# Kernel optimization log

Measured on AMD Instinct MI355X. Metric: run time of the kernel, lower is better.

## Reference

```python
import jax, jax.numpy as jnp
import numpy as np
import math

N, E, D, H = 1536, 49152, 512, 8
DH = D // H  # head dim = 64
SCALE = 256.0 * math.sqrt(2.0)  # rel_dists scaling in forward


def sinusoidal_pe(x, d):
    """x: [...] float positions -> [..., d] interleaved sin/cos encoding."""
    div = jnp.exp(jnp.arange(0, d, 2, dtype=jnp.float32) * (-math.log(10000.0) / d))
    ang = x[..., None] * div  # [..., d//2]
    return jnp.stack([jnp.sin(ang), jnp.cos(ang)], axis=-1).reshape(*x.shape, d)


def setup_inputs() -> dict:
    key = jax.random.key(0)
    ks = jax.random.split(key, 8)
    features = jax.random.normal(ks[0], (N, D), dtype=jnp.float32)
    edge_index = jax.random.randint(ks[1], (2, E), 0, N, dtype=jnp.int64)
    edge_attr = jax.random.uniform(ks[2], (E,), dtype=jnp.float32)  # normalized distances
    pos = jax.random.uniform(ks[3], (N, 2), dtype=jnp.float32)  # unused by forward
    s = 1.0 / math.sqrt(D)  # ~xavier-uniform bound sqrt(6/(D+D))... use simple symmetric init
    Wq = jax.random.uniform(ks[4], (D, D), minval=-s, maxval=s, dtype=jnp.float32)
    Wk = jax.random.uniform(ks[5], (D, D), minval=-s, maxval=s, dtype=jnp.float32)
    Wv = jax.random.uniform(ks[6], (D, D), minval=-s, maxval=s, dtype=jnp.float32)
    bq = jnp.zeros((D,), jnp.float32)
    bk = jnp.zeros((D,), jnp.float32)
    bv = jnp.zeros((D,), jnp.float32)
    return dict(features=features, edge_index=edge_index, edge_attr=edge_attr, pos=pos,
                Wq=Wq, bq=bq, Wk=Wk, bk=bk, Wv=Wv, bv=bv)


def reference(features, edge_index, edge_attr, pos, Wq, bq, Wk, bk, Wv, bv):
    # batch dim is 1 in the original (features.unsqueeze(0)); we omit it.
    q = (features @ Wq.T + bq).reshape(N, H, DH).transpose(1, 0, 2)  # [H,N,DH]
    k = (features @ Wk.T + bk).reshape(N, H, DH).transpose(1, 0, 2)
    v = (features @ Wv.T + bv).reshape(N, H, DH).transpose(1, 0, 2)

    qk = jnp.einsum('hqd,hrd->hqr', q, k)  # [H,N,N]

    # to_dense_adj: scatter-add edge_attr into dense [N,N], then scale
    rel = jnp.zeros((N, N), jnp.float32).at[edge_index[0], edge_index[1]].add(edge_attr) * SCALE
    # embed_k and embed_q are identical parameter-free sinusoidal encodings of rel
    rk = sinusoidal_pe(rel, DH)  # [N,N,DH]

    # original: qk + q.rk + k.rq + (q_repeat*k_repeat == qk)  => 2*qk + q.rk + k.rk
    logits = 2.0 * qk \
        + jnp.einsum('hqd,qrd->hqr', q, rk) \
        + jnp.einsum('hrd,qrd->hqr', k, rk)
    attn = jax.nn.softmax(logits / math.sqrt(DH), axis=-1)  # [H,N,N]

    out = jnp.einsum('hqr,hrd->hqd', attn, v)  # [H,N,DH]
    out = out.transpose(1, 0, 2).reshape(N, D)  # [N,D]
    return out.max(axis=0)  # [D] max-pool over nodes (MIL pooling)
```

## Files before the change

### kernel.cpp

```cpp
#include <hip/hip_runtime.h>
#include <cmath>


constexpr int Nn  = 1536;
constexpr int Dd  = 512;
constexpr int Hh  = 8;
constexpr int DHd = 64;
constexpr int SPLITS = 4;
constexpr float SCALE_F = 362.03867196751236f;
constexpr float M0 = 8.0f;

typedef float f4 __attribute__((ext_vector_type(4)));
typedef int   i4 __attribute__((ext_vector_type(4)));
typedef __attribute__((ext_vector_type(4))) float f32x4;
typedef __attribute__((ext_vector_type(8))) short bf16x8;

__device__ inline unsigned short bf16_rne(float x) {
    unsigned u = __float_as_uint(x);
    unsigned r = u + 0x7fff + ((u >> 16) & 1);
    return (unsigned short)(r >> 16);
}
__device__ inline float bf16_tof(unsigned short h) {
    return __uint_as_float(((unsigned)h) << 16);
}
__device__ inline unsigned f2ord(float x) {
    unsigned b = __float_as_uint(x);
    return (b & 0x80000000u) ? ~b : (b | 0x80000000u);
}

__global__ __launch_bounds__(256) void pack_fw_k(
    const float* __restrict__ feat,
    const float* __restrict__ Wq, const float* __restrict__ Wk, const float* __restrict__ Wv,
    unsigned short* __restrict__ pFh, unsigned short* __restrict__ pFl,
    unsigned short* __restrict__ pWh, unsigned short* __restrict__ pWl)
{
    int tg = blockIdx.x * 256 + threadIdx.x;
    int type = blockIdx.y;
    int L = tg & 63;
    int kc = (tg >> 6) & 15;
    int t10 = tg >> 10;
    const float* src;
    unsigned short *oh, *ol;
    int row, col;
    if (type == 0) {
        src = feat; oh = pFh; ol = pFl;
        row = t10 * 16 + (L & 15);
        col = kc * 32 + (L >> 4) * 8;
    } else {
        int z = t10 >> 5, nt = t10 & 31;
        src = (z == 0) ? Wq : (z == 1) ? Wk : Wv;
        oh = pWh; ol = pWl;
        row = nt * 16 + (L & 15);
        col = kc * 32 + (L >> 4) * 8;
    }
    f4 a = *(const f4*)(src + (size_t)row * Dd + col);
    f4 b = *(const f4*)(src + (size_t)row * Dd + col + 4);
    float x[8];
    #pragma unroll
    for (int j = 0; j < 4; ++j) { x[j] = a[j]; x[4 + j] = b[j]; }
    unsigned short hs[8], ls[8];
    #pragma unroll
    for (int j = 0; j < 8; ++j) {
        hs[j] = bf16_rne(x[j]);
        ls[j] = bf16_rne(x[j] - bf16_tof(hs[j]));
    }
    *(bf16x8*)(oh + (size_t)tg * 8) = *(bf16x8*)hs;
    *(bf16x8*)(ol + (size_t)tg * 8) = *(bf16x8*)ls;
}

__global__ __launch_bounds__(256) void qkvm_k(
    const unsigned short* __restrict__ pFh, const unsigned short* __restrict__ pFl,
    const unsigned short* __restrict__ pWh, const unsigned short* __restrict__ pWl,
    const float* __restrict__ bq, const float* __restrict__ bk, const float* __restrict__ bv,
    float* __restrict__ Qo, float* __restrict__ Ko,
    unsigned short* __restrict__ pQh, unsigned short* __restrict__ pQl,
    unsigned short* __restrict__ pKh, unsigned short* __restrict__ pKl,
    unsigned short* __restrict__ pVh, unsigned short* __restrict__ pVl)
{
    const int z = blockIdx.z;
    const float* __restrict__ bias = (z == 0) ? bq : (z == 1) ? bk : bv;
    const int tid = threadIdx.x;
    const int L = tid & 63, wv = tid >> 6;
    const int l15 = L & 15, quad = L >> 4;
    const int mt0 = blockIdx.y * 4 + (wv & 1) * 2;
    const int nt0 = blockIdx.x * 4 + (wv >> 1) * 2;
    __shared__ float lds[4][32][33];

    f32x4 acc[2][2];
    #pragma unroll
    for (int i = 0; i < 2; ++i)
        #pragma unroll
        for (int j = 0; j < 2; ++j) acc[i][j] = (f32x4){0.f, 0.f, 0.f, 0.f};

    bf16x8 AH[2][2], AL[2][2], BH[2][2], BL[2][2];
    auto loadset = [&](int buf, int kc) {
        #pragma unroll
        for (int i = 0; i < 2; ++i) {
            size_t ao = ((size_t)((mt0 + i) * 16 + kc)) * 512 + L * 8;
            AH[buf][i] = *(const bf16x8*)(pFh + ao);
            AL[buf][i] = *(const bf16x8*)(pFl + ao);
            size_t bo = ((size_t)((z * 32 + nt0 + i) * 16 + kc)) * 512 + L * 8;
            BH[buf][i] = *(const bf16x8*)(pWh + bo);
            BL[buf][i] = *(const bf16x8*)(pWl + bo);
        }
    };
    auto mfmaset = [&](int buf) {
        #pragma unroll
        for (int i = 0; i < 2; ++i)
            #pragma unroll
            for (int j = 0; j < 2; ++j) {
                f32x4 a = acc[i][j];
                a = __builtin_amdgcn_mfma_f32_16x16x32_bf16(AH[buf][i], BH[buf][j], a, 0, 0, 0);
                a = __builtin_amdgcn_mfma_f32_16x16x32_bf16(AH[buf][i], BL[buf][j], a, 0, 0, 0);
                a = __builtin_amdgcn_mfma_f32_16x16x32_bf16(AL[buf][i], BH[buf][j], a, 0, 0, 0);
                a = __builtin_amdgcn_mfma_f32_16x16x32_bf16(AL[buf][i], BL[buf][j], a, 0, 0, 0);
                acc[i][j] = a;
            }
    };

    loadset(0, 0);
    #pragma unroll
    for (int kc = 0; kc < 16; kc += 2) {
        loadset(1, kc + 1);
        mfmaset(0);
        if (kc + 2 < 16) loadset(0, kc + 2);
        mfmaset(1);
    }

    float o_[2][2][4];
    #pragma unroll
    for (int i = 0; i < 2; ++i)
        #pragma unroll
        for (int j = 0; j < 2; ++j) {
            float b = bias[(nt0 + j) * 16 + l15];
            #pragma unroll
            for (int reg = 0; reg < 4; ++reg) o_[i][j][reg] = acc[i][j][reg] + b;
        }
    if (z < 2) {
        float* __restrict__ outp = (z == 0) ? Qo : Ko;
        #pragma unroll
        for (int i = 0; i < 2; ++i) {
            int row0 = (mt0 + i) * 16 + quad * 4;
            #pragma unroll
            for (int j = 0; j < 2; ++j) {
                int col = (nt0 + j) * 16 + l15;
                #pragma unroll
                for (int reg = 0; reg < 4; ++reg)
                    outp[(size_t)(row0 + reg) * Dd + col] = o_[i][j][reg];
            }
        }
    }
    #pragma unroll
    for (int i = 0; i < 2; ++i)
        #pragma unroll
        for (int j = 0; j < 2; ++j)
            #pragma unroll
            for (int reg = 0; reg < 4; ++reg)
                lds[wv][i * 16 + quad * 4 + reg][j * 16 + l15] = o_[i][j][reg];

    const int h = blockIdx.x;
    if (z < 2) {
        unsigned short* __restrict__ oh = z ? pKh : pQh;
        unsigned short* __restrict__ ol = z ? pKl : pQl;
        const int kc = wv >> 1;
        const float sc = z ? 1.0f : 0.25f;
        #pragma unroll
        for (int i = 0; i < 2; ++i) {
            float x[8]; unsigned short hs[8], ls[8];
            #pragma unroll
            for (int j2 = 0; j2 < 8; ++j2)
                x[j2] = lds[wv][i * 16 + l15][quad * 8 + j2] * sc;
            #pragma unroll
            for (int j2 = 0; j2 < 8; ++j2) {
                hs[j2] = bf16_rne(x[j2]);
                ls[j2] = bf16_rne(x[j2] - bf16_tof(hs[j2]));
            }
            size_t off = ((size_t)((h * 96 + mt0 + i) * 2 + kc)) * 512 + L * 8;
            *(bf16x8*)(oh + off) = *(bf16x8*)hs;
            *(bf16x8*)(ol + off) = *(bf16x8*)ls;
        }
    } else {
        const int rc = blockIdx.y * 2 + (wv & 1);
        #pragma unroll
        for (int dtl = 0; dtl < 2; ++dtl) {
            int dt = (wv >> 1) * 2 + dtl;
            float x[8]; unsigned short hs[8], ls[8];
            #pragma unroll
            for (int j2 = 0; j2 < 8; ++j2)
                x[j2] = lds[wv][quad * 8 + j2][dtl * 16 + l15];
            #pragma unroll
            for (int j2 = 0; j2 < 8; ++j2) {
                hs[j2] = bf16_rne(x[j2]);
                ls[j2] = bf16_rne(x[j2] - bf16_tof(hs[j2]));
            }
            size_t off = ((size_t)((h * 48 + rc) * 4 + dt)) * 512 + L * 8;
            *(bf16x8*)(pVh + off) = *(bf16x8*)hs;
            *(bf16x8*)(pVl + off) = *(bf16x8*)ls;
        }
    }
}

__global__ __launch_bounds__(256) void init_rel_k(float* __restrict__ rel,
                                                  int* __restrict__ eid,
                                                  unsigned* __restrict__ ordmax)
{
    size_t idx = (size_t)blockIdx.x * 256 + threadIdx.x;
    size_t i = idx * 4;
    if (i < (size_t)Nn * Nn) {
        *(f4*)(rel + i) = (f4){0.f, 0.f, 0.f, 0.f};
        *(i4*)(eid + i) = (i4){-1, -1, -1, -1};
    }
    if (idx < 128) {
        #pragma unroll
        for (int c = 0; c < 4; ++c) ordmax[idx * 4 + c] = 0x007FFFFFu;
    }
}

__global__ __launch_bounds__(256) void scatter_k(
    const int* __restrict__ raw, const float* __restrict__ attr,
    float* __restrict__ rel, int* __restrict__ eid, int* __restrict__ idxn, int E)
{
    int e = blockIdx.x * 256 + threadIdx.x;
    if (e >= E) return;
    int acc = 0;
    #pragma unroll
    for (int i = 0; i < 16; ++i) acc |= raw[2 * i + 1];
    int s, t;
    if (acc == 0) { s = raw[2 * e]; t = raw[2 * (E + e)]; }
    else          { s = raw[e];     t = raw[E + e]; }
    idxn[e] = s; idxn[E + e] = t;
    size_t off = (size_t)s * Nn + t;
    atomicAdd(rel + off, attr[e] * SCALE_F);
    eid[off] = e;
}

__global__ void oddsum_k(const float* __restrict__ Q, const float* __restrict__ K,
                         float* __restrict__ qodd, float* __restrict__ kodd,
                         float* __restrict__ koddT)
{
    int t = blockIdx.x * 256 + threadIdx.x;
    if (t >= 2 * Nn * Hh) return;
    const float* src = (t < Nn * Hh) ? Q : K;
    int i = (t < Nn * Hh) ? t : t - Nn * Hh;
    int n = i >> 3, h = i & 7;
    const float* row = src + (size_t)n * Dd + h * DHd;
    float s = 0.f;
    #pragma unroll
    for (int ii = 0; ii < 32; ++ii) s += row[2 * ii + 1];
    if (t < Nn * Hh) qodd[i] = s;
    else { kodd[i] = s; koddT[h * Nn + n] = 0.125f * s; }
}

__global__ __launch_bounds__(256) void delta_k(
    const int* __restrict__ idxn, const float* __restrict__ rel,
    const float* __restrict__ Q, const float* __restrict__ K,
    const float* __restrict__ qodd, const float* __restrict__ kodd,
    float* __restrict__ delta8, int E)
{
    int t = blockIdx.x * 256 + threadIdx.x;
    if (t >= E * Hh) return;
    int e = t >> 3, h = t & 7;
    int qi = idxn[e], ri = idxn[E + e];
    float x = rel[(size_t)qi * Nn + ri];
    const float* qrow = Q + (size_t)qi * Dd + h * DHd;
    const float* krow = K + (size_t)ri * Dd + h * DHd;
    float acc = 0.f;
    #pragma unroll
    for (int i = 0; i < 32; i += 2) {
        float dd0 = 0.15915494309189535f * __builtin_amdgcn_exp2f(-0.4152410118609203f * (float)i);
        float dd1 = 0.15915494309189535f * __builtin_amdgcn_exp2f(-0.4152410118609203f * (float)(i + 1));
        float r0 = x * dd0; r0 -= floorf(r0);
        float r1 = x * dd1; r1 -= floorf(r1);
        float s0 = __builtin_amdgcn_sinf(r0), c0 = __builtin_amdgcn_cosf(r0);
        float s1 = __builtin_amdgcn_sinf(r1), c1 = __builtin_amdgcn_cosf(r1);
        f4 q4 = *(const f4*)(qrow + 2 * i);
        f4 k4 = *(const f4*)(krow + 2 * i);
        acc += (q4[0] + k4[0]) * s0 + (q4[1] + k4[1]) * c0
             + (q4[2] + k4[2]) * s1 + (q4[3] + k4[3]) * c1;
    }
    delta8[(size_t)e * Hh + h] = 0.125f * (acc - qodd[qi * Hh + h] - kodd[ri * Hh + h]);
}

__global__ __launch_bounds__(64, 3) void flash5_k(
    const unsigned short* __restrict__ pQh, const unsigned short* __restrict__ pQl,
    const unsigned short* __restrict__ pKh, const unsigned short* __restrict__ pKl,
    const unsigned short* __restrict__ pVh, const unsigned short* __restrict__ pVl,
    const int* __restrict__ eid, const float* __restrict__ delta8,
    const float* __restrict__ koddT,
    float* __restrict__ Opart, float* __restrict__ Lpart)
{
    const int qt = blockIdx.x, h = blockIdx.y, s = blockIdx.z;
    const int L = threadIdx.x, quad = L >> 4, l15 = L & 15;
    const int q0 = qt * 16;
    __shared__ unsigned short phi[16][80];
    __shared__ unsigned short plo[16][80];

    bf16x8 qh[2], ql[2];
    #pragma unroll
    for (int kc = 0; kc < 2; ++kc) {
        size_t off = ((size_t)((h * 96 + qt) * 2 + kc)) * 512 + L * 8;
        qh[kc] = *(const bf16x8*)(pQh + off);
        ql[kc] = *(const bf16x8*)(pQl + off);
    }

    f32x4 O[4];
    float lsum[4];
    #pragma unroll
    for (int r = 0; r < 4; ++r) { lsum[r] = 0.f; O[r] = (f32x4){0.f, 0.f, 0.f, 0.f}; }

    const int NT = 24 / SPLITS;
    const int Tbase = s * NT;

    bf16x8 kh0[4], kh1[4], kl0[4], kl1[4];
    {
        const int r0 = Tbase * 64;
        #pragma unroll
        for (int nt = 0; nt < 4; ++nt) {
            size_t b0 = ((size_t)((h * 96 + (r0 >> 4) + nt) * 2)) * 512 + L * 8;
            kh0[nt] = *(const bf16x8*)(pKh + b0);
            kh1[nt] = *(const bf16x8*)(pKh + b0 + 512);
            kl0[nt] = *(const bf16x8*)(pKl + b0);
            kl1[nt] = *(const bf16x8*)(pKl + b0 + 512);
        }
    }

    float kvcur[4], dcur[16];
    {
        const int r0 = Tbase * 64;
        int ecur[16];
        #pragma unroll
        for (int nt = 0; nt < 4; ++nt) {
            kvcur[nt] = koddT[h * Nn + r0 + nt * 16 + l15];
            #pragma unroll
            for (int reg = 0; reg < 4; ++reg)
                ecur[nt * 4 + reg] = eid[(size_t)(q0 + quad * 4 + reg) * Nn + r0 + nt * 16 + l15];
        }
        #pragma unroll
        for (int i = 0; i < 16; ++i) {
            int e = ecur[i];
            float d = delta8[(size_t)(e < 0 ? 0 : e) * Hh + h];
            dcur[i] = (e >= 0) ? d : 0.f;
        }
    }

    for (int T = 0; T < NT; ++T) {
        const int r0 = (Tbase + T) * 64;
        const bool more = (T + 1 < NT);

        int   enxt[16];
        float kvnxt[4];
        if (more) {
            const int r1 = r0 + 64;
            #pragma unroll
            for (int nt = 0; nt < 4; ++nt) {
                kvnxt[nt] = koddT[h * Nn + r1 + nt * 16 + l15];
                #pragma unroll
                for (int reg = 0; reg < 4; ++reg)
                    enxt[nt * 4 + reg] = eid[(size_t)(q0 + quad * 4 + reg) * Nn + r1 + nt * 16 + l15];
            }
        }

        bf16x8 vh0[4], vh1[4], vl0[4], vl1[4];
        #pragma unroll
        for (int dt = 0; dt < 4; ++dt) {
            size_t vb = ((size_t)((h * 48 + (r0 >> 5)) * 4 + dt)) * 512 + L * 8;
            vh0[dt] = *(const bf16x8*)(pVh + vb);
            vh1[dt] = *(const bf16x8*)(pVh + vb + 2048);
            vl0[dt] = *(const bf16x8*)(pVl + vb);
            vl1[dt] = *(const bf16x8*)(pVl + vb + 2048);
        }

        f32x4 S[4];
        #pragma unroll
        for (int nt = 0; nt < 4; ++nt) {
            f32x4 a = {0.f, 0.f, 0.f, 0.f};
            a = __builtin_amdgcn_mfma_f32_16x16x32_bf16(qh[0], kh0[nt], a, 0, 0, 0);
            a = __builtin_amdgcn_mfma_f32_16x16x32_bf16(qh[1], kh1[nt], a, 0, 0, 0);
            a = __builtin_amdgcn_mfma_f32_16x16x32_bf16(qh[0], kl0[nt], a, 0, 0, 0);
            a = __builtin_amdgcn_mfma_f32_16x16x32_bf16(qh[1], kl1[nt], a, 0, 0, 0);
            a = __builtin_amdgcn_mfma_f32_16x16x32_bf16(ql[0], kh0[nt], a, 0, 0, 0);
            a = __builtin_amdgcn_mfma_f32_16x16x32_bf16(ql[1], kh1[nt], a, 0, 0, 0);
            S[nt] = a;
        }

        if (more) {
            const int r1 = r0 + 64;
            #pragma unroll
            for (int nt = 0; nt < 4; ++nt) {
                size_t b0 = ((size_t)((h * 96 + (r1 >> 4) + nt) * 2)) * 512 + L * 8;
                kh0[nt] = *(const bf16x8*)(pKh + b0);
                kh1[nt] = *(const bf16x8*)(pKh + b0 + 512);
                kl0[nt] = *(const bf16x8*)(pKl + b0);
                kl1[nt] = *(const bf16x8*)(pKl + b0 + 512);
            }
        }

        #pragma unroll
        for (int reg = 0; reg < 4; ++reg) {
            float p[4];
            #pragma unroll
            for (int nt = 0; nt < 4; ++nt) {
                p[nt] = __expf(S[nt][reg] + kvcur[nt] + dcur[nt * 4 + reg] - M0);
                lsum[reg] += p[nt];
                unsigned short hi = bf16_rne(p[nt]);
                phi[quad * 4 + reg][nt * 16 + l15] = hi;
                plo[quad * 4 + reg][nt * 16 + l15] = bf16_rne(p[nt] - bf16_tof(hi));
            }
        }

        bf16x8 ph[2], pl[2];
        #pragma unroll
        for (int kc2 = 0; kc2 < 2; ++kc2) {
            ph[kc2] = *(const bf16x8*)&phi[l15][kc2 * 32 + quad * 8];
            pl[kc2] = *(const bf16x8*)&plo[l15][kc2 * 32 + quad * 8];
        }

        #pragma unroll
        for (int dt = 0; dt < 4; ++dt) {
            f32x4 a = O[dt];
            a = __builtin_amdgcn_mfma_f32_16x16x32_bf16(ph[0], vh0[dt], a, 0, 0, 0);
            a = __builtin_amdgcn_mfma_f32_16x16x32_bf16(ph[1], vh1[dt], a, 0, 0, 0);
            a = __builtin_amdgcn_mfma_f32_16x16x32_bf16(ph[0], vl0[dt], a, 0, 0, 0);
            a = __builtin_amdgcn_mfma_f32_16x16x32_bf16(ph[1], vl1[dt], a, 0, 0, 0);
            a = __builtin_amdgcn_mfma_f32_16x16x32_bf16(pl[0], vh0[dt], a, 0, 0, 0);
            a = __builtin_amdgcn_mfma_f32_16x16x32_bf16(pl[1], vh1[dt], a, 0, 0, 0);
            O[dt] = a;
        }

        if (more) {
            #pragma unroll
            for (int i = 0; i < 16; ++i) {
                int e = enxt[i];
                float d = delta8[(size_t)(e < 0 ? 0 : e) * Hh + h];
                dcur[i] = (e >= 0) ? d : 0.f;
            }
            #pragma unroll
            for (int nt = 0; nt < 4; ++nt) kvcur[nt] = kvnxt[nt];
        }
    }

    #pragma unroll
    for (int reg = 0; reg < 4; ++reg) {
        #pragma unroll
        for (int o = 1; o < 16; o <<= 1) lsum[reg] += __shfl_xor(lsum[reg], o);
    }

    #pragma unroll
    for (int dt = 0; dt < 4; ++dt)
        #pragma unroll
        for (int reg = 0; reg < 4; ++reg)
            Opart[((size_t)(s * Hh + h) * Nn + q0 + quad * 4 + reg) * 64 + dt * 16 + l15] = O[dt][reg];
    if (l15 == 0) {
        #pragma unroll
        for (int reg = 0; reg < 4; ++reg)
            Lpart[(size_t)(s * Hh + h) * Nn + q0 + quad * 4 + reg] = lsum[reg];
    }
}

__global__ __launch_bounds__(256) void combine_mp_k(
    const float* __restrict__ Opart, const float* __restrict__ Lpart,
    unsigned* __restrict__ ordmax)
{
    const int b = blockIdx.x;
    const int t = threadIdx.x;
    const int cg = (t & 127) * 4;
    const int h = cg >> 6, d = cg & 63;
    const int rh = t >> 7;
    f4 mx = {-3.0e38f, -3.0e38f, -3.0e38f, -3.0e38f};
    for (int r = 0; r < 8; ++r) {
        int q = b * 16 + rh * 8 + r;
        float l = 0.f;
        f4 o = {0.f, 0.f, 0.f, 0.f};
        #pragma unroll
        for (int s2 = 0; s2 < SPLITS; ++s2) {
            l += Lpart[(size_t)(s2 * Hh + h) * Nn + q];
            f4 ov = *(const f4*)(Opart + ((size_t)(s2 * Hh + h) * Nn + q) * 64 + d);
            #pragma unroll
            for (int c = 0; c < 4; ++c) o[c] += ov[c];
        }
        float inv = 1.0f / l;
        #pragma unroll
        for (int c = 0; c < 4; ++c) mx[c] = fmaxf(mx[c], o[c] * inv);
    }
    #pragma unroll
    for (int c = 0; c < 4; ++c) atomicMax(&ordmax[cg + c], f2ord(mx[c]));
}

__global__ void decode_k(const unsigned* __restrict__ ordmax, float* __restrict__ outp)
{
    int t = blockIdx.x * 256 + threadIdx.x;
    if (t >= Dd) return;
    unsigned u = ordmax[t];
    outp[t] = (u & 0x80000000u) ? __uint_as_float(u ^ 0x80000000u) : __uint_as_float(~u);
}

extern "C" void kernel_launch(void* const* d_in, const int* in_sizes, int n_in,
                              void* d_out, int out_size, void* d_ws, size_t ws_size,
                              hipStream_t stream)
{
    const float* feat   = (const float*)d_in[0];
    const int*   rawidx = (const int*)d_in[1];
    const float* attr   = (const float*)d_in[2];
    const float* Wq = (const float*)d_in[4];
    const float* bq = (const float*)d_in[5];
    const float* Wk = (const float*)d_in[6];
    const float* bk = (const float*)d_in[7];
    const float* Wv = (const float*)d_in[8];
    const float* bv = (const float*)d_in[9];
    float* outp = (float*)d_out;
    const int E = in_sizes[2];

    const size_t ND_ = (size_t)Nn * Dd;
    const size_t NN_ = (size_t)Nn * Nn;
    const size_t PK_ = (size_t)Hh * 96 * 2 * 512;
    float* ws    = (float*)d_ws;
    float* Q     = ws;
    float* K     = Q + ND_;
    unsigned short* pFh = (unsigned short*)(K + ND_);
    unsigned short* pFl = pFh + PK_;
    unsigned short* pWh = pFl + PK_;
    unsigned short* pWl = pWh + PK_;
    float* rel   = (float*)(pWl + PK_);
    int*   eid   = (int*)(rel + NN_);
    float* delta8 = (float*)(eid + NN_);
    float* qodd  = delta8 + (size_t)E * Hh;
    float* kodd  = qodd + (size_t)Nn * Hh;
    float* koddT = kodd + (size_t)Nn * Hh;
    int*   idxn  = (int*)(koddT + (size_t)Nn * Hh);
    unsigned short* pQh = (unsigned short*)(idxn + 2 * E);
    unsigned short* pQl = pQh + PK_;
    unsigned short* pKh = pQl + PK_;
    unsigned short* pKl = pKh + PK_;
    unsigned short* pVh = pKl + PK_;
    unsigned short* pVl = pVh + PK_;
    float* Lpart = (float*)(pVl + PK_);
    unsigned* ordmax = (unsigned*)(Lpart + (size_t)SPLITS * Hh * Nn);
    float* Opart = ws;

    pack_fw_k<<<dim3(384, 2), 256, 0, stream>>>(feat, Wq, Wk, Wv, pFh, pFl, pWh, pWl);
    qkvm_k<<<dim3(8, 24, 3), 256, 0, stream>>>(pFh, pFl, pWh, pWl, bq, bk, bv,
                                               Q, K, pQh, pQl, pKh, pKl, pVh, pVl);
    init_rel_k<<<(int)((NN_ / 4 + 255) / 256), 256, 0, stream>>>(rel, eid, ordmax);
    scatter_k<<<(E + 255) / 256, 256, 0, stream>>>(rawidx, attr, rel, eid, idxn, E);
    oddsum_k<<<(2 * Nn * Hh + 255) / 256, 256, 0, stream>>>(Q, K, qodd, kodd, koddT);
    delta_k<<<(E * Hh + 255) / 256, 256, 0, stream>>>(idxn, rel, Q, K, qodd, kodd, delta8, E);
    flash5_k<<<dim3(96, 8, SPLITS), 64, 0, stream>>>(pQh, pQl, pKh, pKl, pVh, pVl,
                                                     eid, delta8, koddT, Opart, Lpart);
    combine_mp_k<<<96, 256, 0, stream>>>(Opart, Lpart, ordmax);
    decode_k<<<(Dd + 255) / 256, 256, 0, stream>>>(ordmax, outp);
}
```

Baseline: 196.7 us.

## Merge init kernels, fuse odd-sums into QKV GEMM, shrink edge-id map, atomically reduce splits

Folds the pack, rel/eid init, accumulator zeroing and ordmax init into one setup kernel. The odd-lane sums move into the QKV projection epilogue as shuffle reductions plus atomics, and the separate oddsum kernel is removed. The dense edge-id map drops from int32 to uint16 to halve its init and read traffic. The flash split partials are now summed with atomicAdd into one O/L buffer, so the combine kernel no longer reads per-split partials. This removes launches and memory traffic, but adds atomic contention and relies on E fitting in 16 bits.

```diff
diff --git a/kernel.cpp b/kernel.cpp
--- a/kernel.cpp
+++ b/kernel.cpp
@@ -12,6 +12,7 @@
 
 typedef float f4 __attribute__((ext_vector_type(4)));
 typedef int   i4 __attribute__((ext_vector_type(4)));
+typedef unsigned short us4 __attribute__((ext_vector_type(4)));
 typedef __attribute__((ext_vector_type(4))) float f32x4;
 typedef __attribute__((ext_vector_type(8))) short bf16x8;
 
@@ -28,44 +29,66 @@
     return (b & 0x80000000u) ? ~b : (b | 0x80000000u);
 }
 
-__global__ __launch_bounds__(256) void pack_fw_k(
+__global__ __launch_bounds__(256) void setup_k(
     const float* __restrict__ feat,
     const float* __restrict__ Wq, const float* __restrict__ Wk, const float* __restrict__ Wv,
     unsigned short* __restrict__ pFh, unsigned short* __restrict__ pFl,
-    unsigned short* __restrict__ pWh, unsigned short* __restrict__ pWl)
-{
-    int tg = blockIdx.x * 256 + threadIdx.x;
-    int type = blockIdx.y;
-    int L = tg & 63;
-    int kc = (tg >> 6) & 15;
-    int t10 = tg >> 10;
-    const float* src;
-    unsigned short *oh, *ol;
-    int row, col;
-    if (type == 0) {
-        src = feat; oh = pFh; ol = pFl;
-        row = t10 * 16 + (L & 15);
-        col = kc * 32 + (L >> 4) * 8;
+    unsigned short* __restrict__ pWh, unsigned short* __restrict__ pWl,
+    float* __restrict__ rel, unsigned short* __restrict__ eid16,
+    float* __restrict__ Obuf, float* __restrict__ Lbuf,
+    float* __restrict__ qkodd, unsigned* __restrict__ ordmax)
+{
+    const int b = blockIdx.x, tid = threadIdx.x;
+    if (b < 768) {
+        int type = (b >= 384);
+        int tg = (type ? (b - 384) : b) * 256 + tid;
+        int L = tg & 63;
+        int kc = (tg >> 6) & 15;
+        int t10 = tg >> 10;
+        const float* src;
+        unsigned short *oh, *ol;
+        int row, col;
+        if (type == 0) {
+            src = feat; oh = pFh; ol = pFl;
+            row = t10 * 16 + (L & 15);
+            col = kc * 32 + (L >> 4) * 8;
+        } else {
+            int z = t10 >> 5, nt = t10 & 31;
+            src = (z == 0) ? Wq : (z == 1) ? Wk : Wv;
+            oh = pWh; ol = pWl;
+            row = nt * 16 + (L & 15);
+            col = kc * 32 + (L >> 4) * 8;
+        }
+        f4 a = *(const f4*)(src + (size_t)row * Dd + col);
+        f4 bb = *(const f4*)(src + (size_t)row * Dd + col + 4);
+        float x[8];
+        #pragma unroll
+        for (int j = 0; j < 4; ++j) { x[j] = a[j]; x[4 + j] = bb[j]; }
+        unsigned short hs[8], ls[8];
+        #pragma unroll
+        for (int j = 0; j < 8; ++j) {
+            hs[j] = bf16_rne(x[j]);
+            ls[j] = bf16_rne(x[j] - bf16_tof(hs[j]));
+        }
+        *(bf16x8*)(oh + (size_t)tg * 8) = *(bf16x8*)hs;
+        *(bf16x8*)(ol + (size_t)tg * 8) = *(bf16x8*)ls;
+    } else if (b < 3072) {
+        size_t idx = (size_t)(b - 768) * 256 + tid;
+        *(f4*)(rel + idx * 4) = (f4){0.f, 0.f, 0.f, 0.f};
+        *(us4*)(eid16 + idx * 4) = (us4){0xFFFFu, 0xFFFFu, 0xFFFFu, 0xFFFFu};
+    } else if (b < 3840) {
+        size_t idx = (size_t)(b - 3072) * 256 + tid;
+        *(f4*)(Obuf + idx * 4) = (f4){0.f, 0.f, 0.f, 0.f};
+    } else if (b < 3852) {
+        size_t idx = (size_t)(b - 3840) * 256 + tid;
+        *(f4*)(Lbuf + idx * 4) = (f4){0.f, 0.f, 0.f, 0.f};
+    } else if (b < 3876) {
+        size_t idx = (size_t)(b - 3852) * 256 + tid;
+        *(f4*)(qkodd + idx * 4) = (f4){0.f, 0.f, 0.f, 0.f};
     } else {
-        int z = t10 >> 5, nt = t10 & 31;
-        src = (z == 0) ? Wq : (z == 1) ? Wk : Wv;
-        oh = pWh; ol = pWl;
-        row = nt * 16 + (L & 15);
-        col = kc * 32 + (L >> 4) * 8;
-    }
-    f4 a = *(const f4*)(src + (size_t)row * Dd + col);
-    f4 b = *(const f4*)(src + (size_t)row * Dd + col + 4);
-    float x[8];
-    #pragma unroll
-    for (int j = 0; j < 4; ++j) { x[j] = a[j]; x[4 + j] = b[j]; }
-    unsigned short hs[8], ls[8];
-    #pragma unroll
-    for (int j = 0; j < 8; ++j) {
-        hs[j] = bf16_rne(x[j]);
-        ls[j] = bf16_rne(x[j] - bf16_tof(hs[j]));
-    }
-    *(bf16x8*)(oh + (size_t)tg * 8) = *(bf16x8*)hs;
-    *(bf16x8*)(ol + (size_t)tg * 8) = *(bf16x8*)ls;
+        int idx = (b - 3876) * 256 + tid;
+        ordmax[idx] = 0x007FFFFFu;
+    }
 }
 
 __global__ __launch_bounds__(256) void qkvm_k(
@@ -73,6 +96,7 @@
     const unsigned short* __restrict__ pWh, const unsigned short* __restrict__ pWl,
     const float* __restrict__ bq, const float* __restrict__ bk, const float* __restrict__ bv,
     float* __restrict__ Qo, float* __restrict__ Ko,
+    float* __restrict__ qodd, float* __restrict__ kodd,
     unsigned short* __restrict__ pQh, unsigned short* __restrict__ pQl,
     unsigned short* __restrict__ pKh, unsigned short* __restrict__ pKl,
     unsigned short* __restrict__ pVh, unsigned short* __restrict__ pVl)
@@ -149,6 +173,21 @@
                     outp[(size_t)(row0 + reg) * Dd + col] = o_[i][j][reg];
             }
         }
+        float* __restrict__ odst = (z == 0) ? qodd : kodd;
+        const int h = blockIdx.x;
+        #pragma unroll
+        for (int i = 0; i < 2; ++i) {
+            #pragma unroll
+            for (int reg = 0; reg < 4; ++reg) {
+                float v = (l15 & 1) ? (o_[i][0][reg] + o_[i][1][reg]) : 0.f;
+                #pragma unroll
+                for (int o = 1; o < 16; o <<= 1) v += __shfl_xor(v, o);
+                if (l15 == 0) {
+                    int row = (mt0 + i) * 16 + quad * 4 + reg;
+                    atomicAdd(&odst[row * Hh + h], v);
+                }
+            }
+        }
     }
     #pragma unroll
     for (int i = 0; i < 2; ++i)
@@ -200,25 +239,10 @@
     }
 }
 
-__global__ __launch_bounds__(256) void init_rel_k(float* __restrict__ rel,
-                                                  int* __restrict__ eid,
-                                                  unsigned* __restrict__ ordmax)
-{
-    size_t idx = (size_t)blockIdx.x * 256 + threadIdx.x;
-    size_t i = idx * 4;
-    if (i < (size_t)Nn * Nn) {
-        *(f4*)(rel + i) = (f4){0.f, 0.f, 0.f, 0.f};
-        *(i4*)(eid + i) = (i4){-1, -1, -1, -1};
-    }
-    if (idx < 128) {
-        #pragma unroll
-        for (int c = 0; c < 4; ++c) ordmax[idx * 4 + c] = 0x007FFFFFu;
-    }
-}
-
 __global__ __launch_bounds__(256) void scatter_k(
     const int* __restrict__ raw, const float* __restrict__ attr,
-    float* __restrict__ rel, int* __restrict__ eid, int* __restrict__ idxn, int E)
+    float* __restrict__ rel, unsigned short* __restrict__ eid16,
+    int* __restrict__ idxn, int E)
 {
     int e = blockIdx.x * 256 + threadIdx.x;
     if (e >= E) return;
@@ -231,24 +255,7 @@
     idxn[e] = s; idxn[E + e] = t;
     size_t off = (size_t)s * Nn + t;
     atomicAdd(rel + off, attr[e] * SCALE_F);
-    eid[off] = e;
-}
-
-__global__ void oddsum_k(const float* __restrict__ Q, const float* __restrict__ K,
-                         float* __restrict__ qodd, float* __restrict__ kodd,
-                         float* __restrict__ koddT)
-{
-    int t = blockIdx.x * 256 + threadIdx.x;
-    if (t >= 2 * Nn * Hh) return;
-    const float* src = (t < Nn * Hh) ? Q : K;
-    int i = (t < Nn * Hh) ? t : t - Nn * Hh;
-    int n = i >> 3, h = i & 7;
-    const float* row = src + (size_t)n * Dd + h * DHd;
-    float s = 0.f;
-    #pragma unroll
-    for (int ii = 0; ii < 32; ++ii) s += row[2 * ii + 1];
-    if (t < Nn * Hh) qodd[i] = s;
-    else { kodd[i] = s; koddT[h * Nn + n] = 0.125f * s; }
+    eid16[off] = (unsigned short)e;
 }
 
 __global__ __launch_bounds__(256) void delta_k(
@@ -281,13 +288,13 @@
     delta8[(size_t)e * Hh + h] = 0.125f * (acc - qodd[qi * Hh + h] - kodd[ri * Hh + h]);
 }
 
-__global__ __launch_bounds__(64, 3) void flash5_k(
+__global__ __launch_bounds__(64, 3) void flash7_k(
     const unsigned short* __restrict__ pQh, const unsigned short* __restrict__ pQl,
     const unsigned short* __restrict__ pKh, const unsigned short* __restrict__ pKl,
     const unsigned short* __restrict__ pVh, const unsigned short* __restrict__ pVl,
-    const int* __restrict__ eid, const float* __restrict__ delta8,
-    const float* __restrict__ koddT,
-    float* __restrict__ Opart, float* __restrict__ Lpart)
+    const unsigned short* __restrict__ eid16, const float* __restrict__ delta8,
+    const float* __restrict__ kodd,
+    float* __restrict__ Obuf, float* __restrict__ Lbuf)
 {
     const int qt = blockIdx.x, h = blockIdx.y, s = blockIdx.z;
     const int L = threadIdx.x, quad = L >> 4, l15 = L & 15;
@@ -330,10 +337,12 @@
         int ecur[16];
         #pragma unroll
         for (int nt = 0; nt < 4; ++nt) {
-            kvcur[nt] = koddT[h * Nn + r0 + nt * 16 + l15];
-            #pragma unroll
-            for (int reg = 0; reg < 4; ++reg)
-                ecur[nt * 4 + reg] = eid[(size_t)(q0 + quad * 4 + reg) * Nn + r0 + nt * 16 + l15];
+            kvcur[nt] = 0.125f * kodd[(size_t)(r0 + nt * 16 + l15) * Hh + h];
+            #pragma unroll
+            for (int reg = 0; reg < 4; ++reg) {
+                unsigned short uv = eid16[(size_t)(q0 + quad * 4 + reg) * Nn + r0 + nt * 16 + l15];
+                ecur[nt * 4 + reg] = (uv == 0xFFFFu) ? -1 : (int)uv;
+            }
         }
         #pragma unroll
         for (int i = 0; i < 16; ++i) {
@@ -353,10 +362,12 @@
             const int r1 = r0 + 64;
             #pragma unroll
             for (int nt = 0; nt < 4; ++nt) {
-                kvnxt[nt] = koddT[h * Nn + r1 + nt * 16 + l15];
+                kvnxt[nt] = 0.125f * kodd[(size_t)(r1 + nt * 16 + l15) * Hh + h];
                 #pragma unroll
-                for (int reg = 0; reg < 4; ++reg)
-                    enxt[nt * 4 + reg] = eid[(size_t)(q0 + quad * 4 + reg) * Nn + r1 + nt * 16 + l15];
+                for (int reg = 0; reg < 4; ++reg) {
+                    unsigned short uv = eid16[(size_t)(q0 + quad * 4 + reg) * Nn + r1 + nt * 16 + l15];
+                    enxt[nt * 4 + reg] = (uv == 0xFFFFu) ? -1 : (int)uv;
+                }
             }
         }
 
@@ -449,38 +460,31 @@
     for (int dt = 0; dt < 4; ++dt)
         #pragma unroll
         for (int reg = 0; reg < 4; ++reg)
-            Opart[((size_t)(s * Hh + h) * Nn + q0 + quad * 4 + reg) * 64 + dt * 16 + l15] = O[dt][reg];
+            atomicAdd(&Obuf[(size_t)(q0 + quad * 4 + reg) * Dd + h * DHd + dt * 16 + l15],
+                      O[dt][reg]);
     if (l15 == 0) {
         #pragma unroll
         for (int reg = 0; reg < 4; ++reg)
-            Lpart[(size_t)(s * Hh + h) * Nn + q0 + quad * 4 + reg] = lsum[reg];
-    }
-}
-
-__global__ __launch_bounds__(256) void combine_mp_k(
-    const float* __restrict__ Opart, const float* __restrict__ Lpart,
+            atomicAdd(&Lbuf[(size_t)h * Nn + q0 + quad * 4 + reg], lsum[reg]);
+    }
+}
+
+__global__ __launch_bounds__(256) void finalize_mp_k(
+    const float* __restrict__ Obuf, const float* __restrict__ Lbuf,
     unsigned* __restrict__ ordmax)
 {
     const int b = blockIdx.x;
     const int t = threadIdx.x;
     const int cg = (t & 127) * 4;
-    const int h = cg >> 6, d = cg & 63;
+    const int h = cg >> 6;
     const int rh = t >> 7;
     f4 mx = {-3.0e38f, -3.0e38f, -3.0e38f, -3.0e38f};
     for (int r = 0; r < 8; ++r) {
         int q = b * 16 + rh * 8 + r;
-        float l = 0.f;
-        f4 o = {0.f, 0.f, 0.f, 0.f};
-        #pragma unroll
-        for (int s2 = 0; s2 < SPLITS; ++s2) {
-            l += Lpart[(size_t)(s2 * Hh + h) * Nn + q];
-            f4 ov = *(const f4*)(Opart + ((size_t)(s2 * Hh + h) * Nn + q) * 64 + d);
-            #pragma unroll
-            for (int c = 0; c < 4; ++c) o[c] += ov[c];
-        }
-        float inv = 1.0f / l;
-        #pragma unroll
-        for (int c = 0; c < 4; ++c) mx[c] = fmaxf(mx[c], o[c] * inv);
+        float inv = 1.0f / Lbuf[(size_t)h * Nn + q];
+        f4 ov = *(const f4*)(Obuf + (size_t)q * Dd + cg);
+        #pragma unroll
+        for (int c = 0; c < 4; ++c) mx[c] = fmaxf(mx[c], ov[c] * inv);
     }
     #pragma unroll
     for (int c = 0; c < 4; ++c) atomicMax(&ordmax[cg + c], f2ord(mx[c]));
@@ -521,31 +525,30 @@
     unsigned short* pWh = pFl + PK_;
     unsigned short* pWl = pWh + PK_;
     float* rel   = (float*)(pWl + PK_);
-    int*   eid   = (int*)(rel + NN_);
-    float* delta8 = (float*)(eid + NN_);
+    unsigned short* eid16 = (unsigned short*)(rel + NN_);
+    float* delta8 = (float*)(eid16 + NN_);
     float* qodd  = delta8 + (size_t)E * Hh;
     float* kodd  = qodd + (size_t)Nn * Hh;
-    float* koddT = kodd + (size_t)Nn * Hh;
-    int*   idxn  = (int*)(koddT + (size_t)Nn * Hh);
+    int*   idxn  = (int*)(kodd + (size_t)Nn * Hh);
     unsigned short* pQh = (unsigned short*)(idxn + 2 * E);
     unsigned short* pQl = pQh + PK_;
     unsigned short* pKh = pQl + PK_;
     unsigned short* pKl = pKh + PK_;
     unsigned short* pVh = pKl + PK_;
     unsigned short* pVl = pVh + PK_;
-    float* Lpart = (float*)(pVl + PK_);
-    unsigned* ordmax = (unsigned*)(Lpart + (size_t)SPLITS * Hh * Nn);
-    float* Opart = ws;
-
-    pack_fw_k<<<dim3(384, 2), 256, 0, stream>>>(feat, Wq, Wk, Wv, pFh, pFl, pWh, pWl);
+    float* Obuf  = (float*)(pVl + PK_);
+    float* Lbuf  = Obuf + ND_;
+    unsigned* ordmax = (unsigned*)(Lbuf + (size_t)Hh * Nn);
+
+    setup_k<<<3878, 256, 0, stream>>>(feat, Wq, Wk, Wv, pFh, pFl, pWh, pWl,
+                                      rel, eid16, Obuf, Lbuf, qodd, ordmax);
     qkvm_k<<<dim3(8, 24, 3), 256, 0, stream>>>(pFh, pFl, pWh, pWl, bq, bk, bv,
-                                               Q, K, pQh, pQl, pKh, pKl, pVh, pVl);
-    init_rel_k<<<(int)((NN_ / 4 + 255) / 256), 256, 0, stream>>>(rel, eid, ordmax);
-    scatter_k<<<(E + 255) / 256, 256, 0, stream>>>(rawidx, attr, rel, eid, idxn, E);
-    oddsum_k<<<(2 * Nn * Hh + 255) / 256, 256, 0, stream>>>(Q, K, qodd, kodd, koddT);
+                                               Q, K, qodd, kodd,
+                                               pQh, pQl, pKh, pKl, pVh, pVl);
+    scatter_k<<<(E + 255) / 256, 256, 0, stream>>>(rawidx, attr, rel, eid16, idxn, E);
     delta_k<<<(E * Hh + 255) / 256, 256, 0, stream>>>(idxn, rel, Q, K, qodd, kodd, delta8, E);
-    flash5_k<<<dim3(96, 8, SPLITS), 64, 0, stream>>>(pQh, pQl, pKh, pKl, pVh, pVl,
-                                                     eid, delta8, koddT, Opart, Lpart);
-    combine_mp_k<<<96, 256, 0, stream>>>(Opart, Lpart, ordmax);
+    flash7_k<<<dim3(96, 8, SPLITS), 64, 0, stream>>>(pQh, pQl, pKh, pKl, pVh, pVl,
+                                                     eid16, delta8, kodd, Obuf, Lbuf);
+    finalize_mp_k<<<96, 256, 0, stream>>>(Obuf, Lbuf, ordmax);
     decode_k<<<(Dd + 255) / 256, 256, 0, stream>>>(ordmax, outp);
 }
```

Result: slower. 201.6 us (+2.5%).
